# Performance work log

Hardware: AMD Instinct MI355X
Metric: run time of the kernel (lower is better)

The kernel has to match this reference:

```python
import jax, jax.numpy as jnp
import numpy as np

D_MODEL, D_STATE, D_CONV, EXPAND = 1024, 16, 4, 2
D_INNER = D_MODEL * EXPAND
B, L = 2, 2048


def setup_inputs() -> dict:
    key = jax.random.key(0)
    ks = jax.random.split(key, 12)
    s = lambda *sh: 1.0 / np.sqrt(sh[-1])
    x = jax.random.normal(ks[0], (B, L, D_MODEL), dtype=jnp.float32)
    W_in = jax.random.normal(ks[1], (2 * D_INNER, D_MODEL), dtype=jnp.float32) * s(D_MODEL)
    conv_w = jax.random.normal(ks[2], (D_INNER, 1, D_CONV), dtype=jnp.float32) * s(D_CONV)
    conv_b = jax.random.normal(ks[3], (D_INNER,), dtype=jnp.float32) * 0.01
    W_x = jax.random.normal(ks[4], (2 * D_STATE, D_INNER), dtype=jnp.float32) * s(D_INNER)
    W_dt = jax.random.normal(ks[5], (D_INNER, D_INNER), dtype=jnp.float32) * s(D_INNER)
    b_dt = jax.random.normal(ks[6], (D_INNER,), dtype=jnp.float32) * 0.01
    A_log = jnp.log(jnp.broadcast_to(jnp.arange(1, D_STATE + 1, dtype=jnp.float32)[None, :], (D_INNER, D_STATE)))
    Dp = jnp.ones((D_INNER,), dtype=jnp.float32)
    W_out = jax.random.normal(ks[7], (D_MODEL, D_INNER), dtype=jnp.float32) * s(D_INNER)
    ln_g = jnp.ones((D_MODEL,), dtype=jnp.float32)
    ln_b = jnp.zeros((D_MODEL,), dtype=jnp.float32)
    return {"x": x, "W_in": W_in, "conv_w": conv_w, "conv_b": conv_b, "W_x": W_x,
            "W_dt": W_dt, "b_dt": b_dt, "A_log": A_log, "Dp": Dp, "W_out": W_out,
            "ln_g": ln_g, "ln_b": ln_b}


def _layernorm(x, g, b, eps=1e-5):
    mu = jnp.mean(x, axis=-1, keepdims=True)
    var = jnp.mean(jnp.square(x - mu), axis=-1, keepdims=True)
    return (x - mu) * jax.lax.rsqrt(var + eps) * g + b


def _silu(x):
    return x * jax.nn.sigmoid(x)


def _ssm(x, A_log, Dp, W_x, W_dt, b_dt):
    # x: (B, L, D_INNER)
    A = -jnp.exp(A_log)                                  # (D, N)
    x_dbl = jnp.einsum('bld,nd->bln', x, W_x)            # (B, L, 2N)
    B_mat, C_mat = jnp.split(x_dbl, 2, axis=-1)          # (B, L, N) each
    dt = jax.nn.softplus(jnp.einsum('bld,ed->ble', x, W_dt) + b_dt)  # (B, L, D)

    def step(h, inp):
        dt_t, B_t, C_t, x_t = inp                        # (B,D),(B,N),(B,N),(B,D)
        A_bar = jnp.exp(dt_t[..., None] * A)             # (B, D, N)
        h = A_bar * h + (dt_t * x_t)[..., None] * B_t[:, None, :]
        y_t = jnp.einsum('bdn,bn->bd', h, C_t)
        return h, y_t

    h0 = jnp.zeros((x.shape[0], D_INNER, D_STATE), dtype=x.dtype)
    xs = (jnp.swapaxes(dt, 0, 1), jnp.swapaxes(B_mat, 0, 1),
          jnp.swapaxes(C_mat, 0, 1), jnp.swapaxes(x, 0, 1))
    _, ys = jax.lax.scan(step, h0, xs)                   # ys: (L, B, D)
    y = jnp.swapaxes(ys, 0, 1)
    return y + Dp * x


def reference(x, W_in, conv_w, conv_b, W_x, W_dt, b_dt, A_log, Dp, W_out, ln_g, ln_b):
    residual = x
    xn = _layernorm(x, ln_g, ln_b)
    xz = jnp.einsum('bld,ed->ble', xn, W_in)             # (B, L, 2*D_INNER)
    x_branch, z = jnp.split(xz, 2, axis=-1)
    # causal depthwise conv1d (torch pads both sides then truncates to L == left pad)
    x_c = jax.lax.conv_general_dilated(
        jnp.swapaxes(x_branch, 1, 2), conv_w,
        window_strides=(1,), padding=[(D_CONV - 1, 0)],
        dimension_numbers=('NCH', 'OIH', 'NCH'),
        feature_group_count=D_INNER) + conv_b[None, :, None]
    x_branch = _silu(jnp.swapaxes(x_c, 1, 2))
    y = _ssm(x_branch, A_log, Dp, W_x, W_dt, b_dt)
    y = y * _silu(z)
    return jnp.einsum('bld,md->blm', y, W_out) + residual
```

## Files before the change

kernel.cpp:

```cpp
#include <hip/hip_runtime.h>
#include <math.h>

#define D_MODEL 1024
#define D_STATE 16
#define D_INNER 2048
#define BATCH 2
#define SEQ 2048
#define ROWS (BATCH * SEQ)
#define NCAT (D_INNER + 2 * D_STATE)

#define CHUNK 32
#define NCH (SEQ / CHUNK)

typedef __bf16 bf16x8 __attribute__((ext_vector_type(8)));
typedef float f32x4 __attribute__((ext_vector_type(4)));

__device__ __forceinline__ unsigned short f2bf(float f) {
    unsigned u = __float_as_uint(f);
    u += 0x7FFF + ((u >> 16) & 1);
    return (unsigned short)(u >> 16);
}
__device__ __forceinline__ float bf2f(unsigned short s) {
    return __uint_as_float((unsigned)s << 16);
}
__device__ __forceinline__ float fast_softplus(float x) {
    return x > 15.f ? x : __logf(1.f + __expf(x));
}

__global__ __launch_bounds__(256) void ln_kernel(const float* __restrict__ x,
                                                 const float* __restrict__ g,
                                                 const float* __restrict__ b,
                                                 unsigned short* __restrict__ out) {
    int r = blockIdx.x;
    int t = threadIdx.x;
    const float* xr = x + (size_t)r * D_MODEL;
    float4 v = *(const float4*)(xr + t * 4);
    float s  = v.x + v.y + v.z + v.w;
    float ss = v.x * v.x + v.y * v.y + v.z * v.z + v.w * v.w;
    for (int off = 32; off > 0; off >>= 1) {
        s  += __shfl_down(s, off);
        ss += __shfl_down(ss, off);
    }
    __shared__ float ws[8], wss[8];
    int wid = t >> 6, lane = t & 63;
    if (lane == 0) { ws[wid] = s; wss[wid] = ss; }
    __syncthreads();
    if (t == 0) {
        float S = 0.f, SS = 0.f;
        for (int i = 0; i < 4; ++i) { S += ws[i]; SS += wss[i]; }
        float mu = S * (1.f / D_MODEL);
        float var = SS * (1.f / D_MODEL) - mu * mu;
        ws[4] = mu;
        ws[5] = rsqrtf(var + 1e-5f);
    }
    __syncthreads();
    float mu = ws[4], rs = ws[5];
    float4 gv = *(const float4*)(g + t * 4);
    float4 bv = *(const float4*)(b + t * 4);
    ushort4 o;
    o.x = f2bf((v.x - mu) * rs * gv.x + bv.x);
    o.y = f2bf((v.y - mu) * rs * gv.y + bv.y);
    o.z = f2bf((v.z - mu) * rs * gv.z + bv.z);
    o.w = f2bf((v.w - mu) * rs * gv.w + bv.w);
    ((ushort4*)(out + (size_t)r * D_MODEL))[t] = o;
}

#define N4_WIN  (2 * D_INNER * D_MODEL / 4)
#define N4_WDT  (D_INNER * D_INNER / 4)
#define N4_WX   (2 * D_STATE * D_INNER / 4)
#define N4_WOUT (D_MODEL * D_INNER / 4)
#define N4_ALL  (N4_WIN + N4_WDT + N4_WX + N4_WOUT)

__global__ __launch_bounds__(256) void cast_weights(const float* __restrict__ W_in,
                                                    const float* __restrict__ W_dt,
                                                    const float* __restrict__ W_x,
                                                    const float* __restrict__ W_out,
                                                    unsigned short* __restrict__ Win_b,
                                                    unsigned short* __restrict__ Wcat_b,
                                                    unsigned short* __restrict__ Wout_b) {
    int i = blockIdx.x * 256 + threadIdx.x;
    const float* src;
    unsigned short* dst;
    int j = i;
    if (j < N4_WIN) { src = W_in; dst = Win_b; }
    else if ((j -= N4_WIN) < N4_WDT) { src = W_dt; dst = Wcat_b; }
    else if ((j -= N4_WDT) < N4_WX)  { src = W_x;  dst = Wcat_b + (size_t)D_INNER * D_INNER; }
    else if ((j -= N4_WX) < N4_WOUT) { src = W_out; dst = Wout_b; }
    else return;
    float4 v = ((const float4*)src)[j];
    ushort4 o;
    o.x = f2bf(v.x); o.y = f2bf(v.y); o.z = f2bf(v.z); o.w = f2bf(v.w);
    ((ushort4*)dst)[j] = o;
}

template <bool BF16_OUT>
__global__ __launch_bounds__(256) void gemm_mfma(const unsigned short* __restrict__ A,
                                                 const unsigned short* __restrict__ Bw,
                                                 void* __restrict__ Cv,
                                                 const float* __restrict__ resid,
                                                 int M, int N, int K, int nby) {
    __shared__ unsigned short As[2][128 * 32];
    __shared__ unsigned short Bs[2][128 * 32];
    const int t = threadIdx.x;
    const int wave = t >> 6, lane = t & 63;
    const int bx = blockIdx.x / nby, by = blockIdx.x % nby;
    const int bm = by * 128, bn = bx * 128;
    const int wm = (wave >> 1) * 64, wn = (wave & 1) * 64;

    const int srow0 = 32 * wave;
    const int sr = lane >> 2;
    const int ss = lane & 3;
    const int sc = ss ^ ((sr >> 1) & 3);

    const int mrow = lane & 15, q = lane >> 4;
    const int rslot = q ^ ((mrow >> 1) & 3);

    f32x4 acc[4][4] = {};

    for (int k0 = 0; k0 < K; k0 += 64) {
#pragma unroll
        for (int h = 0; h < 2; ++h) {
#pragma unroll
            for (int j = 0; j < 2; ++j) {
                int r = srow0 + 16 * j + sr;
                const unsigned short* ga = A + (size_t)(bm + r) * K + k0 + 32 * h + sc * 8;
                __builtin_amdgcn_global_load_lds(
                    (const __attribute__((address_space(1))) void*)ga,
                    (__attribute__((address_space(3))) void*)&As[h][(srow0 + 16 * j) * 32],
                    16, 0, 0);
                int nr = bn + r; if (nr > N - 1) nr = N - 1;
                const unsigned short* gb = Bw + (size_t)nr * K + k0 + 32 * h + sc * 8;
                __builtin_amdgcn_global_load_lds(
                    (const __attribute__((address_space(1))) void*)gb,
                    (__attribute__((address_space(3))) void*)&Bs[h][(srow0 + 16 * j) * 32],
                    16, 0, 0);
            }
        }
        __syncthreads();
#pragma unroll
        for (int h = 0; h < 2; ++h) {
            bf16x8 a[4], b[4];
            const bf16x8* Av = (const bf16x8*)As[h];
            const bf16x8* Bv = (const bf16x8*)Bs[h];
#pragma unroll
            for (int i = 0; i < 4; ++i) a[i] = Av[(wm + i * 16 + mrow) * 4 + rslot];
#pragma unroll
            for (int j = 0; j < 4; ++j) b[j] = Bv[(wn + j * 16 + mrow) * 4 + rslot];
#pragma unroll
            for (int i = 0; i < 4; ++i)
#pragma unroll
                for (int j = 0; j < 4; ++j)
                    acc[i][j] = __builtin_amdgcn_mfma_f32_16x16x32_bf16(a[i], b[j], acc[i][j], 0, 0, 0);
        }
        __syncthreads();
    }

#pragma unroll
    for (int j = 0; j < 4; ++j) {
        int col = bn + wn + j * 16 + mrow;
        if (col < N) {
#pragma unroll
            for (int i = 0; i < 4; ++i) {
                int rowb = bm + wm + i * 16 + q * 4;
#pragma unroll
                for (int r = 0; r < 4; ++r) {
                    size_t idx = (size_t)(rowb + r) * N + col;
                    float v = acc[i][j][r];
                    if (BF16_OUT) {
                        ((unsigned short*)Cv)[idx] = f2bf(v);
                    } else {
                        if (resid) v += resid[idx];
                        ((float*)Cv)[idx] = v;
                    }
                }
            }
        }
    }
}

__global__ __launch_bounds__(256) void conv_silu(const unsigned short* __restrict__ xz_b,
                                                 const float* __restrict__ cw,
                                                 const float* __restrict__ cb,
                                                 unsigned short* __restrict__ out_b) {
    int idx = blockIdx.x * 256 + threadIdx.x;
    int d4 = (idx & (D_INNER / 4 - 1)) * 4;
    int r = idx >> 9;
    int l = r & (SEQ - 1);
    const unsigned short* base = xz_b + (size_t)r * (2 * D_INNER) + d4;
    float4 b4 = *(const float4*)(cb + d4);
    float acc[4] = {b4.x, b4.y, b4.z, b4.w};
    ushort4 xq[4];
#pragma unroll
    for (int j = 0; j < 4; ++j)
        if (l >= 3 - j) xq[j] = *(const ushort4*)(base - (size_t)(3 - j) * (2 * D_INNER));
#pragma unroll
    for (int i = 0; i < 4; ++i) {
        float4 w = *(const float4*)(cw + (size_t)(d4 + i) * 4);
        const float* wp = (const float*)&w;
#pragma unroll
        for (int j = 0; j < 4; ++j) {
            if (l >= 3 - j) {
                unsigned short q = (&xq[j].x)[i];
                acc[i] = fmaf(wp[j], bf2f(q), acc[i]);
            }
        }
    }
    ushort4 o;
#pragma unroll
    for (int i = 0; i < 4; ++i) {
        float sv = acc[i] / (1.f + __expf(-acc[i]));
        (&o.x)[i] = f2bf(sv);
    }
    *(ushort4*)(out_b + (size_t)r * D_INNER + d4) = o;
}

__global__ __launch_bounds__(256) void scan_pass1(const float* __restrict__ dtcat,
                                                  const unsigned short* __restrict__ xconv_b,
                                                  const float* __restrict__ b_dt,
                                                  float* __restrict__ hfin,
                                                  float* __restrict__ Ssum) {
    int blk = blockIdx.x;
    int dblk = blk & 7;
    int b = (blk >> 3) & (BATCH - 1);
    int c = blk >> 4;
    int t = threadIdx.x;
    int d = dblk * 256 + t;
    int r0 = b * SEQ + c * CHUNK;

    __shared__ float bcs[CHUNK][32];
    {
        int row = t >> 3, f4 = t & 7;
        const float4* src = (const float4*)(dtcat + (size_t)(r0 + row) * NCAT + D_INNER);
        *(float4*)&bcs[row][f4 * 4] = src[f4];
    }
    __syncthreads();

    float h[D_STATE] = {};
    float S = 0.f;
    float bdt = b_dt[d];
    float dtp = dtcat[(size_t)r0 * NCAT + d];
    unsigned short xq = xconv_b[(size_t)r0 * D_INNER + d];
    for (int l = 0; l < CHUNK; ++l) {
        float dtp_n = 0.f; unsigned short xq_n = 0;
        if (l + 1 < CHUNK) {
            dtp_n = dtcat[(size_t)(r0 + l + 1) * NCAT + d];
            xq_n = xconv_b[(size_t)(r0 + l + 1) * D_INNER + d];
        }
        float dtv = fast_softplus(dtp + bdt);
        S += dtv;
        float dtx = dtv * bf2f(xq);
        float w = __expf(-dtv);
        float ab = 1.f;
#pragma unroll
        for (int n = 0; n < D_STATE; ++n) {
            ab *= w;
            h[n] = fmaf(ab, h[n], dtx * bcs[l][n]);
        }
        dtp = dtp_n; xq = xq_n;
    }
    size_t cb = ((size_t)c * BATCH + b);
#pragma unroll
    for (int n = 0; n < D_STATE; ++n)
        hfin[(cb * D_STATE + n) * D_INNER + d] = h[n];
    Ssum[cb * D_INNER + d] = S;
}

__global__ __launch_bounds__(256) void scan_pass2(const float* __restrict__ hfin,
                                                  const float* __restrict__ Ssum,
                                                  const float* __restrict__ A_log,
                                                  float* __restrict__ Hinit) {
    int tid = blockIdx.x * 256 + threadIdx.x;
    int d = tid & (D_INNER - 1);
    int n = (tid >> 11) & (D_STATE - 1);
    int b = tid >> 15;
    float Ac = -__expf(A_log[(size_t)d * D_STATE + n]);
    float H = 0.f;
    for (int c = 0; c < NCH; ++c) {
        size_t cb = ((size_t)c * BATCH + b);
        size_t idx = (cb * D_STATE + n) * D_INNER + d;
        Hinit[idx] = H;
        float s = Ssum[cb * D_INNER + d];
        H = fmaf(__expf(Ac * s), H, hfin[idx]);
    }
}

__global__ __launch_bounds__(256) void scan_pass3(const float* __restrict__ dtcat,
                                                  const unsigned short* __restrict__ xconv_b,
                                                  const unsigned short* __restrict__ xz_b,
                                                  const float* __restrict__ b_dt,
                                                  const float* __restrict__ Dp,
                                                  const float* __restrict__ Hinit,
                                                  unsigned short* __restrict__ y_b) {
    int blk = blockIdx.x;
    int dblk = blk & 7;
    int b = (blk >> 3) & (BATCH - 1);
    int c = blk >> 4;
    int t = threadIdx.x;
    int d = dblk * 256 + t;
    int r0 = b * SEQ + c * CHUNK;

    __shared__ float bcs[CHUNK][32];
    {
        int row = t >> 3, f4 = t & 7;
        const float4* src = (const float4*)(dtcat + (size_t)(r0 + row) * NCAT + D_INNER);
        *(float4*)&bcs[row][f4 * 4] = src[f4];
    }
    __syncthreads();

    float h[D_STATE];
    size_t cb = ((size_t)c * BATCH + b);
#pragma unroll
    for (int n = 0; n < D_STATE; ++n)
        h[n] = Hinit[(cb * D_STATE + n) * D_INNER + d];
    float bdt = b_dt[d];
    float dp = Dp[d];
    float dtp = dtcat[(size_t)r0 * NCAT + d];
    unsigned short xq = xconv_b[(size_t)r0 * D_INNER + d];
    unsigned short zq = xz_b[(size_t)r0 * (2 * D_INNER) + D_INNER + d];
    for (int l = 0; l < CHUNK; ++l) {
        int r = r0 + l;
        float dtp_n = 0.f; unsigned short xq_n = 0, zq_n = 0;
        if (l + 1 < CHUNK) {
            dtp_n = dtcat[(size_t)(r + 1) * NCAT + d];
            xq_n = xconv_b[(size_t)(r + 1) * D_INNER + d];
            zq_n = xz_b[(size_t)(r + 1) * (2 * D_INNER) + D_INNER + d];
        }
        float dtv = fast_softplus(dtp + bdt);
        float xv = bf2f(xq);
        float dtx = dtv * xv;
        float w = __expf(-dtv);
        float ab = 1.f;
        float y = 0.f;
#pragma unroll
        for (int n = 0; n < D_STATE; ++n) {
            ab *= w;
            h[n] = fmaf(ab, h[n], dtx * bcs[l][n]);
            y = fmaf(h[n], bcs[l][D_STATE + n], y);
        }
        y = fmaf(dp, xv, y);
        float zv = bf2f(zq);
        float sz = zv / (1.f + __expf(-zv));
        y_b[(size_t)r * D_INNER + d] = f2bf(y * sz);
        dtp = dtp_n; xq = xq_n; zq = zq_n;
    }
}

extern "C" void kernel_launch(void* const* d_in, const int* in_sizes, int n_in,
                              void* d_out, int out_size, void* d_ws, size_t ws_size,
                              hipStream_t stream) {
    const float* x      = (const float*)d_in[0];
    const float* W_in   = (const float*)d_in[1];
    const float* conv_w = (const float*)d_in[2];
    const float* conv_b = (const float*)d_in[3];
    const float* W_x    = (const float*)d_in[4];
    const float* W_dt   = (const float*)d_in[5];
    const float* b_dt   = (const float*)d_in[6];
    const float* A_log  = (const float*)d_in[7];
    const float* Dp     = (const float*)d_in[8];
    const float* W_out  = (const float*)d_in[9];
    const float* ln_g   = (const float*)d_in[10];
    const float* ln_b   = (const float*)d_in[11];
    float* out = (float*)d_out;

    unsigned short* xz_b = (unsigned short*)d_ws;
    float* dtcat = (float*)(xz_b + (size_t)ROWS * 2 * D_INNER);
    unsigned short* xn_b    = (unsigned short*)(dtcat + (size_t)ROWS * NCAT);
    unsigned short* Win_b   = xn_b   + (size_t)2 * D_INNER * D_MODEL;
    unsigned short* Wcat_b  = Win_b  + (size_t)2 * D_INNER * D_MODEL;
    unsigned short* Wout_b  = Wcat_b + (size_t)NCAT * D_INNER;
    unsigned short* xconv_b = Wout_b + (size_t)D_MODEL * D_INNER;
    unsigned short* y_b     = xconv_b;
    float* hfin  = (float*)(xconv_b + (size_t)ROWS * D_INNER);
    float* Hinit = hfin + (size_t)NCH * BATCH * D_STATE * D_INNER;
    float* Ssum  = Hinit + (size_t)NCH * BATCH * D_STATE * D_INNER;

    cast_weights<<<(N4_ALL + 255) / 256, 256, 0, stream>>>(
        W_in, W_dt, W_x, W_out, Win_b, Wcat_b, Wout_b);
    ln_kernel<<<ROWS, 256, 0, stream>>>(x, ln_g, ln_b, xn_b);

    gemm_mfma<true><<<32 * 32, 256, 0, stream>>>(xn_b, Win_b, xz_b, nullptr,
                                                 ROWS, 2 * D_INNER, D_MODEL, 32);

    conv_silu<<<(ROWS * D_INNER / 4) / 256, 256, 0, stream>>>(xz_b, conv_w, conv_b, xconv_b);

    gemm_mfma<false><<<17 * 32, 256, 0, stream>>>(xconv_b, Wcat_b, dtcat, nullptr,
                                                  ROWS, NCAT, D_INNER, 32);

    scan_pass1<<<NCH * BATCH * 8, 256, 0, stream>>>(dtcat, xconv_b, b_dt, hfin, Ssum);
    scan_pass2<<<(BATCH * D_STATE * D_INNER) / 256, 256, 0, stream>>>(hfin, Ssum, A_log, Hinit);
    scan_pass3<<<NCH * BATCH * 8, 256, 0, stream>>>(dtcat, xconv_b, xz_b, b_dt, Dp, Hinit, y_b);

    gemm_mfma<false><<<8 * 32, 256, 0, stream>>>(y_b, Wout_b, out, x,
                                                 ROWS, D_MODEL, D_INNER, 32);
}
```

Before: 375.8 us.

## Register-prefetch double-buffered GEMM pipeline and merge weight cast with layernorm

New measurement: 682.1 us. 1.82x slower.

```diff
diff --git a/kernel.cpp b/kernel.cpp
--- a/kernel.cpp
+++ b/kernel.cpp
@@ -27,12 +27,42 @@
     return x > 15.f ? x : __logf(1.f + __expf(x));
 }
 
-__global__ __launch_bounds__(256) void ln_kernel(const float* __restrict__ x,
-                                                 const float* __restrict__ g,
-                                                 const float* __restrict__ b,
-                                                 unsigned short* __restrict__ out) {
-    int r = blockIdx.x;
+#define N4_WIN  (2 * D_INNER * D_MODEL / 4)
+#define N4_WDT  (D_INNER * D_INNER / 4)
+#define N4_WX   (2 * D_STATE * D_INNER / 4)
+#define N4_WOUT (D_MODEL * D_INNER / 4)
+#define N4_ALL  (N4_WIN + N4_WDT + N4_WX + N4_WOUT)
+#define NCAST_BLK (N4_ALL / 256)
+
+__global__ __launch_bounds__(256) void cast_ln(const float* __restrict__ W_in,
+                                               const float* __restrict__ W_dt,
+                                               const float* __restrict__ W_x,
+                                               const float* __restrict__ W_out,
+                                               unsigned short* __restrict__ Win_b,
+                                               unsigned short* __restrict__ Wcat_b,
+                                               unsigned short* __restrict__ Wout_b,
+                                               const float* __restrict__ x,
+                                               const float* __restrict__ g,
+                                               const float* __restrict__ b,
+                                               unsigned short* __restrict__ xn_b) {
+    __shared__ float ws[8], wss[8];
     int t = threadIdx.x;
+    if (blockIdx.x < NCAST_BLK) {
+        int i = blockIdx.x * 256 + t;
+        const float* src;
+        unsigned short* dst;
+        int j = i;
+        if (j < N4_WIN) { src = W_in; dst = Win_b; }
+        else if ((j -= N4_WIN) < N4_WDT) { src = W_dt; dst = Wcat_b; }
+        else if ((j -= N4_WDT) < N4_WX)  { src = W_x;  dst = Wcat_b + (size_t)D_INNER * D_INNER; }
+        else { j -= N4_WX; src = W_out; dst = Wout_b; }
+        float4 v = ((const float4*)src)[j];
+        ushort4 o;
+        o.x = f2bf(v.x); o.y = f2bf(v.y); o.z = f2bf(v.z); o.w = f2bf(v.w);
+        ((ushort4*)dst)[j] = o;
+        return;
+    }
+    int r = blockIdx.x - NCAST_BLK;
     const float* xr = x + (size_t)r * D_MODEL;
     float4 v = *(const float4*)(xr + t * 4);
     float s  = v.x + v.y + v.z + v.w;
@@ -41,7 +71,6 @@
         s  += __shfl_down(s, off);
         ss += __shfl_down(ss, off);
     }
-    __shared__ float ws[8], wss[8];
     int wid = t >> 6, lane = t & 63;
     if (lane == 0) { ws[wid] = s; wss[wid] = ss; }
     __syncthreads();
@@ -62,35 +91,7 @@
     o.y = f2bf((v.y - mu) * rs * gv.y + bv.y);
     o.z = f2bf((v.z - mu) * rs * gv.z + bv.z);
     o.w = f2bf((v.w - mu) * rs * gv.w + bv.w);
-    ((ushort4*)(out + (size_t)r * D_MODEL))[t] = o;
-}
-
-#define N4_WIN  (2 * D_INNER * D_MODEL / 4)
-#define N4_WDT  (D_INNER * D_INNER / 4)
-#define N4_WX   (2 * D_STATE * D_INNER / 4)
-#define N4_WOUT (D_MODEL * D_INNER / 4)
-#define N4_ALL  (N4_WIN + N4_WDT + N4_WX + N4_WOUT)
-
-__global__ __launch_bounds__(256) void cast_weights(const float* __restrict__ W_in,
-                                                    const float* __restrict__ W_dt,
-                                                    const float* __restrict__ W_x,
-                                                    const float* __restrict__ W_out,
-                                                    unsigned short* __restrict__ Win_b,
-                                                    unsigned short* __restrict__ Wcat_b,
-                                                    unsigned short* __restrict__ Wout_b) {
-    int i = blockIdx.x * 256 + threadIdx.x;
-    const float* src;
-    unsigned short* dst;
-    int j = i;
-    if (j < N4_WIN) { src = W_in; dst = Win_b; }
-    else if ((j -= N4_WIN) < N4_WDT) { src = W_dt; dst = Wcat_b; }
-    else if ((j -= N4_WDT) < N4_WX)  { src = W_x;  dst = Wcat_b + (size_t)D_INNER * D_INNER; }
-    else if ((j -= N4_WX) < N4_WOUT) { src = W_out; dst = Wout_b; }
-    else return;
-    float4 v = ((const float4*)src)[j];
-    ushort4 o;
-    o.x = f2bf(v.x); o.y = f2bf(v.y); o.z = f2bf(v.z); o.w = f2bf(v.w);
-    ((ushort4*)dst)[j] = o;
+    ((ushort4*)(xn_b + (size_t)r * D_MODEL))[t] = o;
 }
 
 template <bool BF16_OUT>
@@ -99,8 +100,8 @@
                                                  void* __restrict__ Cv,
                                                  const float* __restrict__ resid,
                                                  int M, int N, int K, int nby) {
-    __shared__ unsigned short As[2][128 * 32];
-    __shared__ unsigned short Bs[2][128 * 32];
+    __shared__ __align__(16) unsigned short As[2][2][128 * 32];
+    __shared__ __align__(16) unsigned short Bs[2][2][128 * 32];
     const int t = threadIdx.x;
     const int wave = t >> 6, lane = t & 63;
     const int bx = blockIdx.x / nby, by = blockIdx.x % nby;
@@ -115,33 +116,41 @@
     const int mrow = lane & 15, q = lane >> 4;
     const int rslot = q ^ ((mrow >> 1) & 3);
 
+    const unsigned short* Ab = A + (size_t)(bm + srow0 + sr) * K + sc * 8;
+    const size_t arow = (size_t)16 * K;
+    int nr0 = bn + srow0 + sr;      if (nr0 > N - 1) nr0 = N - 1;
+    int nr1 = bn + srow0 + 16 + sr; if (nr1 > N - 1) nr1 = N - 1;
+    const unsigned short* Bb0 = Bw + (size_t)nr0 * K + sc * 8;
+    const unsigned short* Bb1 = Bw + (size_t)nr1 * K + sc * 8;
+
+    uint4 ra[2][8];
+
+    auto load = [&](int set, int k0) {
+#pragma unroll
+        for (int h = 0; h < 2; ++h) {
+            ra[set][h * 2 + 0] = *(const uint4*)(Ab + k0 + 32 * h);
+            ra[set][h * 2 + 1] = *(const uint4*)(Ab + arow + k0 + 32 * h);
+            ra[set][4 + h * 2 + 0] = *(const uint4*)(Bb0 + k0 + 32 * h);
+            ra[set][4 + h * 2 + 1] = *(const uint4*)(Bb1 + k0 + 32 * h);
+        }
+    };
+    auto store = [&](int set, int buf) {
+#pragma unroll
+        for (int h = 0; h < 2; ++h)
+#pragma unroll
+            for (int j = 0; j < 2; ++j) {
+                *(uint4*)(&As[buf][h][(srow0 + 16 * j) * 32 + lane * 8]) = ra[set][h * 2 + j];
+                *(uint4*)(&Bs[buf][h][(srow0 + 16 * j) * 32 + lane * 8]) = ra[set][4 + h * 2 + j];
+            }
+    };
+
     f32x4 acc[4][4] = {};
-
-    for (int k0 = 0; k0 < K; k0 += 64) {
-#pragma unroll
-        for (int h = 0; h < 2; ++h) {
-#pragma unroll
-            for (int j = 0; j < 2; ++j) {
-                int r = srow0 + 16 * j + sr;
-                const unsigned short* ga = A + (size_t)(bm + r) * K + k0 + 32 * h + sc * 8;
-                __builtin_amdgcn_global_load_lds(
-                    (const __attribute__((address_space(1))) void*)ga,
-                    (__attribute__((address_space(3))) void*)&As[h][(srow0 + 16 * j) * 32],
-                    16, 0, 0);
-                int nr = bn + r; if (nr > N - 1) nr = N - 1;
-                const unsigned short* gb = Bw + (size_t)nr * K + k0 + 32 * h + sc * 8;
-                __builtin_amdgcn_global_load_lds(
-                    (const __attribute__((address_space(1))) void*)gb,
-                    (__attribute__((address_space(3))) void*)&Bs[h][(srow0 + 16 * j) * 32],
-                    16, 0, 0);
-            }
-        }
-        __syncthreads();
+    auto compute = [&](int buf) {
 #pragma unroll
         for (int h = 0; h < 2; ++h) {
             bf16x8 a[4], b[4];
-            const bf16x8* Av = (const bf16x8*)As[h];
-            const bf16x8* Bv = (const bf16x8*)Bs[h];
+            const bf16x8* Av = (const bf16x8*)As[buf][h];
+            const bf16x8* Bv = (const bf16x8*)Bs[buf][h];
 #pragma unroll
             for (int i = 0; i < 4; ++i) a[i] = Av[(wm + i * 16 + mrow) * 4 + rslot];
 #pragma unroll
@@ -151,6 +160,26 @@
 #pragma unroll
                 for (int j = 0; j < 4; ++j)
                     acc[i][j] = __builtin_amdgcn_mfma_f32_16x16x32_bf16(a[i], b[j], acc[i][j], 0, 0, 0);
+        }
+    };
+
+    const int nk = K >> 6;
+    load(0, 0);
+    store(0, 0);
+    load(1, 64);
+    __syncthreads();
+
+    for (int i = 0; i < nk; i += 2) {
+        compute(0);
+        {
+            store(1, 1);
+            if (i + 2 < nk) load(0, (i + 2) << 6);
+        }
+        __syncthreads();
+        compute(1);
+        if (i + 2 < nk) {
+            store(0, 0);
+            if (i + 3 < nk) load(1, (i + 3) << 6);
         }
         __syncthreads();
     }
@@ -200,8 +229,8 @@
 #pragma unroll
         for (int j = 0; j < 4; ++j) {
             if (l >= 3 - j) {
-                unsigned short q = (&xq[j].x)[i];
-                acc[i] = fmaf(wp[j], bf2f(q), acc[i]);
+                unsigned short qv = (&xq[j].x)[i];
+                acc[i] = fmaf(wp[j], bf2f(qv), acc[i]);
             }
         }
     }
@@ -374,9 +403,8 @@
     float* Hinit = hfin + (size_t)NCH * BATCH * D_STATE * D_INNER;
     float* Ssum  = Hinit + (size_t)NCH * BATCH * D_STATE * D_INNER;
 
-    cast_weights<<<(N4_ALL + 255) / 256, 256, 0, stream>>>(
-        W_in, W_dt, W_x, W_out, Win_b, Wcat_b, Wout_b);
-    ln_kernel<<<ROWS, 256, 0, stream>>>(x, ln_g, ln_b, xn_b);
+    cast_ln<<<NCAST_BLK + ROWS, 256, 0, stream>>>(
+        W_in, W_dt, W_x, W_out, Win_b, Wcat_b, Wout_b, x, ln_g, ln_b, xn_b);
 
     gemm_mfma<true><<<32 * 32, 256, 0, stream>>>(xn_b, Win_b, xz_b, nullptr,
                                                  ROWS, 2 * D_INNER, D_MODEL, 32);
```

## Merge weight cast with layernorm and add register-prefetch pipelined GEMM for dt projection

Applied to the files above, without the earlier changes.

Result: slower. 537.2 us (+43.0%).

```diff
diff --git a/kernel.cpp b/kernel.cpp
--- a/kernel.cpp
+++ b/kernel.cpp
@@ -27,12 +27,42 @@
     return x > 15.f ? x : __logf(1.f + __expf(x));
 }
 
-__global__ __launch_bounds__(256) void ln_kernel(const float* __restrict__ x,
-                                                 const float* __restrict__ g,
-                                                 const float* __restrict__ b,
-                                                 unsigned short* __restrict__ out) {
-    int r = blockIdx.x;
+#define N4_WIN  (2 * D_INNER * D_MODEL / 4)
+#define N4_WDT  (D_INNER * D_INNER / 4)
+#define N4_WX   (2 * D_STATE * D_INNER / 4)
+#define N4_WOUT (D_MODEL * D_INNER / 4)
+#define N4_ALL  (N4_WIN + N4_WDT + N4_WX + N4_WOUT)
+#define NCAST_BLK (N4_ALL / 256)
+
+__global__ __launch_bounds__(256) void cast_ln(const float* __restrict__ W_in,
+                                               const float* __restrict__ W_dt,
+                                               const float* __restrict__ W_x,
+                                               const float* __restrict__ W_out,
+                                               unsigned short* __restrict__ Win_b,
+                                               unsigned short* __restrict__ Wcat_b,
+                                               unsigned short* __restrict__ Wout_b,
+                                               const float* __restrict__ x,
+                                               const float* __restrict__ g,
+                                               const float* __restrict__ b,
+                                               unsigned short* __restrict__ xn_b) {
+    __shared__ float ws[8], wss[8];
     int t = threadIdx.x;
+    if (blockIdx.x < NCAST_BLK) {
+        int i = blockIdx.x * 256 + t;
+        const float* src;
+        unsigned short* dst;
+        int j = i;
+        if (j < N4_WIN) { src = W_in; dst = Win_b; }
+        else if ((j -= N4_WIN) < N4_WDT) { src = W_dt; dst = Wcat_b; }
+        else if ((j -= N4_WDT) < N4_WX)  { src = W_x;  dst = Wcat_b + (size_t)D_INNER * D_INNER; }
+        else { j -= N4_WX; src = W_out; dst = Wout_b; }
+        float4 v = ((const float4*)src)[j];
+        ushort4 o;
+        o.x = f2bf(v.x); o.y = f2bf(v.y); o.z = f2bf(v.z); o.w = f2bf(v.w);
+        ((ushort4*)dst)[j] = o;
+        return;
+    }
+    int r = blockIdx.x - NCAST_BLK;
     const float* xr = x + (size_t)r * D_MODEL;
     float4 v = *(const float4*)(xr + t * 4);
     float s  = v.x + v.y + v.z + v.w;
@@ -41,7 +71,6 @@
         s  += __shfl_down(s, off);
         ss += __shfl_down(ss, off);
     }
-    __shared__ float ws[8], wss[8];
     int wid = t >> 6, lane = t & 63;
     if (lane == 0) { ws[wid] = s; wss[wid] = ss; }
     __syncthreads();
@@ -62,43 +91,15 @@
     o.y = f2bf((v.y - mu) * rs * gv.y + bv.y);
     o.z = f2bf((v.z - mu) * rs * gv.z + bv.z);
     o.w = f2bf((v.w - mu) * rs * gv.w + bv.w);
-    ((ushort4*)(out + (size_t)r * D_MODEL))[t] = o;
-}
-
-#define N4_WIN  (2 * D_INNER * D_MODEL / 4)
-#define N4_WDT  (D_INNER * D_INNER / 4)
-#define N4_WX   (2 * D_STATE * D_INNER / 4)
-#define N4_WOUT (D_MODEL * D_INNER / 4)
-#define N4_ALL  (N4_WIN + N4_WDT + N4_WX + N4_WOUT)
-
-__global__ __launch_bounds__(256) void cast_weights(const float* __restrict__ W_in,
-                                                    const float* __restrict__ W_dt,
-                                                    const float* __restrict__ W_x,
-                                                    const float* __restrict__ W_out,
-                                                    unsigned short* __restrict__ Win_b,
-                                                    unsigned short* __restrict__ Wcat_b,
-                                                    unsigned short* __restrict__ Wout_b) {
-    int i = blockIdx.x * 256 + threadIdx.x;
-    const float* src;
-    unsigned short* dst;
-    int j = i;
-    if (j < N4_WIN) { src = W_in; dst = Win_b; }
-    else if ((j -= N4_WIN) < N4_WDT) { src = W_dt; dst = Wcat_b; }
-    else if ((j -= N4_WDT) < N4_WX)  { src = W_x;  dst = Wcat_b + (size_t)D_INNER * D_INNER; }
-    else if ((j -= N4_WX) < N4_WOUT) { src = W_out; dst = Wout_b; }
-    else return;
-    float4 v = ((const float4*)src)[j];
-    ushort4 o;
-    o.x = f2bf(v.x); o.y = f2bf(v.y); o.z = f2bf(v.z); o.w = f2bf(v.w);
-    ((ushort4*)dst)[j] = o;
+    ((ushort4*)(xn_b + (size_t)r * D_MODEL))[t] = o;
 }
 
 template <bool BF16_OUT>
-__global__ __launch_bounds__(256) void gemm_mfma(const unsigned short* __restrict__ A,
-                                                 const unsigned short* __restrict__ Bw,
-                                                 void* __restrict__ Cv,
-                                                 const float* __restrict__ resid,
-                                                 int M, int N, int K, int nby) {
+__global__ __launch_bounds__(256) void gemm_dma(const unsigned short* __restrict__ A,
+                                                const unsigned short* __restrict__ Bw,
+                                                void* __restrict__ Cv,
+                                                const float* __restrict__ resid,
+                                                int M, int N, int K, int nby) {
     __shared__ unsigned short As[2][128 * 32];
     __shared__ unsigned short Bs[2][128 * 32];
     const int t = threadIdx.x;
@@ -178,6 +179,119 @@
     }
 }
 
+#define GLOAD(rs, k0)                                                   \
+    {                                                                   \
+        _Pragma("unroll")                                               \
+        for (int h = 0; h < 2; ++h) {                                   \
+            rs[h * 2 + 0] = *(const uint4*)(Ab + (k0) + 32 * h);        \
+            rs[h * 2 + 1] = *(const uint4*)(Ab + arow + (k0) + 32 * h); \
+            rs[4 + h * 2 + 0] = *(const uint4*)(Bb0 + (k0) + 32 * h);   \
+            rs[4 + h * 2 + 1] = *(const uint4*)(Bb1 + (k0) + 32 * h);   \
+        }                                                               \
+    }
+
+#define SSTORE(rs, buf)                                                           \
+    {                                                                             \
+        _Pragma("unroll")                                                         \
+        for (int h = 0; h < 2; ++h) {                                             \
+            *(uint4*)(&As[buf][h][(srow0) * 32 + lane * 8]) = rs[h * 2 + 0];      \
+            *(uint4*)(&As[buf][h][(srow0 + 16) * 32 + lane * 8]) = rs[h * 2 + 1]; \
+            *(uint4*)(&Bs[buf][h][(srow0) * 32 + lane * 8]) = rs[4 + h * 2 + 0];  \
+            *(uint4*)(&Bs[buf][h][(srow0 + 16) * 32 + lane * 8]) = rs[4 + h * 2 + 1]; \
+        }                                                                         \
+    }
+
+#define COMPUTE(buf)                                                              \
+    {                                                                             \
+        _Pragma("unroll")                                                         \
+        for (int h = 0; h < 2; ++h) {                                             \
+            bf16x8 a[4], b[4];                                                    \
+            const bf16x8* Av = (const bf16x8*)As[buf][h];                         \
+            const bf16x8* Bv = (const bf16x8*)Bs[buf][h];                         \
+            _Pragma("unroll")                                                     \
+            for (int i = 0; i < 4; ++i) a[i] = Av[(wm + i * 16 + mrow) * 4 + rslot]; \
+            _Pragma("unroll")                                                     \
+            for (int j = 0; j < 4; ++j) b[j] = Bv[(wn + j * 16 + mrow) * 4 + rslot]; \
+            _Pragma("unroll")                                                     \
+            for (int i = 0; i < 4; ++i)                                           \
+                _Pragma("unroll")                                                 \
+                for (int j = 0; j < 4; ++j)                                       \
+                    acc[i][j] = __builtin_amdgcn_mfma_f32_16x16x32_bf16(a[i], b[j], acc[i][j], 0, 0, 0); \
+        }                                                                         \
+    }
+
+template <bool BF16_OUT>
+__global__ __launch_bounds__(256, 2) void gemm_pipe(const unsigned short* __restrict__ A,
+                                                    const unsigned short* __restrict__ Bw,
+                                                    void* __restrict__ Cv,
+                                                    const float* __restrict__ resid,
+                                                    int M, int N, int K, int nby) {
+    __shared__ __align__(16) unsigned short As[2][2][128 * 32];
+    __shared__ __align__(16) unsigned short Bs[2][2][128 * 32];
+    const int t = threadIdx.x;
+    const int wave = t >> 6, lane = t & 63;
+    const int bx = blockIdx.x / nby, by = blockIdx.x % nby;
+    const int bm = by * 128, bn = bx * 128;
+    const int wm = (wave >> 1) * 64, wn = (wave & 1) * 64;
+
+    const int srow0 = 32 * wave;
+    const int sr = lane >> 2;
+    const int ss = lane & 3;
+    const int sc = ss ^ ((sr >> 1) & 3);
+
+    const int mrow = lane & 15, q = lane >> 4;
+    const int rslot = q ^ ((mrow >> 1) & 3);
+
+    const unsigned short* Ab = A + (size_t)(bm + srow0 + sr) * K + sc * 8;
+    const size_t arow = (size_t)16 * K;
+    int nr0 = bn + srow0 + sr;      if (nr0 > N - 1) nr0 = N - 1;
+    int nr1 = bn + srow0 + 16 + sr; if (nr1 > N - 1) nr1 = N - 1;
+    const unsigned short* Bb0 = Bw + (size_t)nr0 * K + sc * 8;
+    const unsigned short* Bb1 = Bw + (size_t)nr1 * K + sc * 8;
+
+    uint4 r0[8], r1[8];
+    f32x4 acc[4][4] = {};
+
+    const int nk = K >> 6;
+    GLOAD(r0, 0)
+    SSTORE(r0, 0)
+    GLOAD(r1, 64)
+    __syncthreads();
+
+    for (int i = 0; i < nk; i += 2) {
+        if (i + 2 < nk) GLOAD(r0, (i + 2) << 6)
+        COMPUTE(0)
+        SSTORE(r1, 1)
+        __syncthreads();
+        if (i + 3 < nk) GLOAD(r1, (i + 3) << 6)
+        COMPUTE(1)
+        if (i + 2 < nk) SSTORE(r0, 0)
+        __syncthreads();
+    }
+
+#pragma unroll
+    for (int j = 0; j < 4; ++j) {
+        int col = bn + wn + j * 16 + mrow;
+        if (col < N) {
+#pragma unroll
+            for (int i = 0; i < 4; ++i) {
+                int rowb = bm + wm + i * 16 + q * 4;
+#pragma unroll
+                for (int r = 0; r < 4; ++r) {
+                    size_t idx = (size_t)(rowb + r) * N + col;
+                    float v = acc[i][j][r];
+                    if (BF16_OUT) {
+                        ((unsigned short*)Cv)[idx] = f2bf(v);
+                    } else {
+                        if (resid) v += resid[idx];
+                        ((float*)Cv)[idx] = v;
+                    }
+                }
+            }
+        }
+    }
+}
+
 __global__ __launch_bounds__(256) void conv_silu(const unsigned short* __restrict__ xz_b,
                                                  const float* __restrict__ cw,
                                                  const float* __restrict__ cb,
@@ -200,8 +314,8 @@
 #pragma unroll
         for (int j = 0; j < 4; ++j) {
             if (l >= 3 - j) {
-                unsigned short q = (&xq[j].x)[i];
-                acc[i] = fmaf(wp[j], bf2f(q), acc[i]);
+                unsigned short qv = (&xq[j].x)[i];
+                acc[i] = fmaf(wp[j], bf2f(qv), acc[i]);
             }
         }
     }
@@ -374,22 +488,21 @@
     float* Hinit = hfin + (size_t)NCH * BATCH * D_STATE * D_INNER;
     float* Ssum  = Hinit + (size_t)NCH * BATCH * D_STATE * D_INNER;
 
-    cast_weights<<<(N4_ALL + 255) / 256, 256, 0, stream>>>(
-        W_in, W_dt, W_x, W_out, Win_b, Wcat_b, Wout_b);
-    ln_kernel<<<ROWS, 256, 0, stream>>>(x, ln_g, ln_b, xn_b);
-
-    gemm_mfma<true><<<32 * 32, 256, 0, stream>>>(xn_b, Win_b, xz_b, nullptr,
-                                                 ROWS, 2 * D_INNER, D_MODEL, 32);
+    cast_ln<<<NCAST_BLK + ROWS, 256, 0, stream>>>(
+        W_in, W_dt, W_x, W_out, Win_b, Wcat_b, Wout_b, x, ln_g, ln_b, xn_b);
+
+    gemm_dma<true><<<32 * 32, 256, 0, stream>>>(xn_b, Win_b, xz_b, nullptr,
+                                                ROWS, 2 * D_INNER, D_MODEL, 32);
 
     conv_silu<<<(ROWS * D_INNER / 4) / 256, 256, 0, stream>>>(xz_b, conv_w, conv_b, xconv_b);
 
-    gemm_mfma<false><<<17 * 32, 256, 0, stream>>>(xconv_b, Wcat_b, dtcat, nullptr,
+    gemm_pipe<false><<<17 * 32, 256, 0, stream>>>(xconv_b, Wcat_b, dtcat, nullptr,
                                                   ROWS, NCAT, D_INNER, 32);
 
     scan_pass1<<<NCH * BATCH * 8, 256, 0, stream>>>(dtcat, xconv_b, b_dt, hfin, Ssum);
     scan_pass2<<<(BATCH * D_STATE * D_INNER) / 256, 256, 0, stream>>>(hfin, Ssum, A_log, Hinit);
     scan_pass3<<<NCH * BATCH * 8, 256, 0, stream>>>(dtcat, xconv_b, xz_b, b_dt, Dp, Hinit, y_b);
 
-    gemm_mfma<false><<<8 * 32, 256, 0, stream>>>(y_b, Wout_b, out, x,
-                                                 ROWS, D_MODEL, D_INNER, 32);
-}
+    gemm_dma<false><<<8 * 32, 256, 0, stream>>>(y_b, Wout_b, out, x,
+                                                ROWS, D_MODEL, D_INNER, 32);
+}
```

## Merge weight cast with layernorm and store dt projection in bf16

Applied to the files above, without the earlier changes.

Result: no change. 369.8 us (-1.6%).

```diff
diff --git a/kernel.cpp b/kernel.cpp
--- a/kernel.cpp
+++ b/kernel.cpp
@@ -27,12 +27,42 @@
     return x > 15.f ? x : __logf(1.f + __expf(x));
 }
 
-__global__ __launch_bounds__(256) void ln_kernel(const float* __restrict__ x,
-                                                 const float* __restrict__ g,
-                                                 const float* __restrict__ b,
-                                                 unsigned short* __restrict__ out) {
-    int r = blockIdx.x;
+#define N4_WIN  (2 * D_INNER * D_MODEL / 4)
+#define N4_WDT  (D_INNER * D_INNER / 4)
+#define N4_WX   (2 * D_STATE * D_INNER / 4)
+#define N4_WOUT (D_MODEL * D_INNER / 4)
+#define N4_ALL  (N4_WIN + N4_WDT + N4_WX + N4_WOUT)
+#define NCAST_BLK (N4_ALL / 256)
+
+__global__ __launch_bounds__(256) void cast_ln(const float* __restrict__ W_in,
+                                               const float* __restrict__ W_dt,
+                                               const float* __restrict__ W_x,
+                                               const float* __restrict__ W_out,
+                                               unsigned short* __restrict__ Win_b,
+                                               unsigned short* __restrict__ Wcat_b,
+                                               unsigned short* __restrict__ Wout_b,
+                                               const float* __restrict__ x,
+                                               const float* __restrict__ g,
+                                               const float* __restrict__ b,
+                                               unsigned short* __restrict__ xn_b) {
+    __shared__ float ws[8], wss[8];
     int t = threadIdx.x;
+    if (blockIdx.x < NCAST_BLK) {
+        int i = blockIdx.x * 256 + t;
+        const float* src;
+        unsigned short* dst;
+        int j = i;
+        if (j < N4_WIN) { src = W_in; dst = Win_b; }
+        else if ((j -= N4_WIN) < N4_WDT) { src = W_dt; dst = Wcat_b; }
+        else if ((j -= N4_WDT) < N4_WX)  { src = W_x;  dst = Wcat_b + (size_t)D_INNER * D_INNER; }
+        else { j -= N4_WX; src = W_out; dst = Wout_b; }
+        float4 v = ((const float4*)src)[j];
+        ushort4 o;
+        o.x = f2bf(v.x); o.y = f2bf(v.y); o.z = f2bf(v.z); o.w = f2bf(v.w);
+        ((ushort4*)dst)[j] = o;
+        return;
+    }
+    int r = blockIdx.x - NCAST_BLK;
     const float* xr = x + (size_t)r * D_MODEL;
     float4 v = *(const float4*)(xr + t * 4);
     float s  = v.x + v.y + v.z + v.w;
@@ -41,7 +71,6 @@
         s  += __shfl_down(s, off);
         ss += __shfl_down(ss, off);
     }
-    __shared__ float ws[8], wss[8];
     int wid = t >> 6, lane = t & 63;
     if (lane == 0) { ws[wid] = s; wss[wid] = ss; }
     __syncthreads();
@@ -62,43 +91,15 @@
     o.y = f2bf((v.y - mu) * rs * gv.y + bv.y);
     o.z = f2bf((v.z - mu) * rs * gv.z + bv.z);
     o.w = f2bf((v.w - mu) * rs * gv.w + bv.w);
-    ((ushort4*)(out + (size_t)r * D_MODEL))[t] = o;
-}
-
-#define N4_WIN  (2 * D_INNER * D_MODEL / 4)
-#define N4_WDT  (D_INNER * D_INNER / 4)
-#define N4_WX   (2 * D_STATE * D_INNER / 4)
-#define N4_WOUT (D_MODEL * D_INNER / 4)
-#define N4_ALL  (N4_WIN + N4_WDT + N4_WX + N4_WOUT)
-
-__global__ __launch_bounds__(256) void cast_weights(const float* __restrict__ W_in,
-                                                    const float* __restrict__ W_dt,
-                                                    const float* __restrict__ W_x,
-                                                    const float* __restrict__ W_out,
-                                                    unsigned short* __restrict__ Win_b,
-                                                    unsigned short* __restrict__ Wcat_b,
-                                                    unsigned short* __restrict__ Wout_b) {
-    int i = blockIdx.x * 256 + threadIdx.x;
-    const float* src;
-    unsigned short* dst;
-    int j = i;
-    if (j < N4_WIN) { src = W_in; dst = Win_b; }
-    else if ((j -= N4_WIN) < N4_WDT) { src = W_dt; dst = Wcat_b; }
-    else if ((j -= N4_WDT) < N4_WX)  { src = W_x;  dst = Wcat_b + (size_t)D_INNER * D_INNER; }
-    else if ((j -= N4_WX) < N4_WOUT) { src = W_out; dst = Wout_b; }
-    else return;
-    float4 v = ((const float4*)src)[j];
-    ushort4 o;
-    o.x = f2bf(v.x); o.y = f2bf(v.y); o.z = f2bf(v.z); o.w = f2bf(v.w);
-    ((ushort4*)dst)[j] = o;
-}
-
-template <bool BF16_OUT>
-__global__ __launch_bounds__(256) void gemm_mfma(const unsigned short* __restrict__ A,
-                                                 const unsigned short* __restrict__ Bw,
-                                                 void* __restrict__ Cv,
-                                                 const float* __restrict__ resid,
-                                                 int M, int N, int K, int nby) {
+    ((ushort4*)(xn_b + (size_t)r * D_MODEL))[t] = o;
+}
+
+template <int MODE>
+__global__ __launch_bounds__(256) void gemm_dma(const unsigned short* __restrict__ A,
+                                                const unsigned short* __restrict__ Bw,
+                                                void* __restrict__ Cv,
+                                                float* __restrict__ aux,
+                                                int M, int N, int K, int nby) {
     __shared__ unsigned short As[2][128 * 32];
     __shared__ unsigned short Bs[2][128 * 32];
     const int t = threadIdx.x;
@@ -164,13 +165,18 @@
                 int rowb = bm + wm + i * 16 + q * 4;
 #pragma unroll
                 for (int r = 0; r < 4; ++r) {
-                    size_t idx = (size_t)(rowb + r) * N + col;
                     float v = acc[i][j][r];
-                    if (BF16_OUT) {
-                        ((unsigned short*)Cv)[idx] = f2bf(v);
+                    if (MODE == 1) {
+                        ((unsigned short*)Cv)[(size_t)(rowb + r) * N + col] = f2bf(v);
+                    } else if (MODE == 0) {
+                        size_t idx = (size_t)(rowb + r) * N + col;
+                        if (aux) v += aux[idx];
+                        ((float*)Cv)[idx] = v;
                     } else {
-                        if (resid) v += resid[idx];
-                        ((float*)Cv)[idx] = v;
+                        if (col < D_INNER)
+                            ((unsigned short*)Cv)[(size_t)(rowb + r) * D_INNER + col] = f2bf(v);
+                        else
+                            aux[(size_t)(rowb + r) * (2 * D_STATE) + (col - D_INNER)] = v;
                     }
                 }
             }
@@ -200,8 +206,8 @@
 #pragma unroll
         for (int j = 0; j < 4; ++j) {
             if (l >= 3 - j) {
-                unsigned short q = (&xq[j].x)[i];
-                acc[i] = fmaf(wp[j], bf2f(q), acc[i]);
+                unsigned short qv = (&xq[j].x)[i];
+                acc[i] = fmaf(wp[j], bf2f(qv), acc[i]);
             }
         }
     }
@@ -214,7 +220,8 @@
     *(ushort4*)(out_b + (size_t)r * D_INNER + d4) = o;
 }
 
-__global__ __launch_bounds__(256) void scan_pass1(const float* __restrict__ dtcat,
+__global__ __launch_bounds__(256) void scan_pass1(const unsigned short* __restrict__ dtb,
+                                                  const float* __restrict__ xdbl,
                                                   const unsigned short* __restrict__ xconv_b,
                                                   const float* __restrict__ b_dt,
                                                   float* __restrict__ hfin,
@@ -228,25 +235,21 @@
     int r0 = b * SEQ + c * CHUNK;
 
     __shared__ float bcs[CHUNK][32];
-    {
-        int row = t >> 3, f4 = t & 7;
-        const float4* src = (const float4*)(dtcat + (size_t)(r0 + row) * NCAT + D_INNER);
-        *(float4*)&bcs[row][f4 * 4] = src[f4];
-    }
+    ((float4*)&bcs[0][0])[t] = ((const float4*)(xdbl + (size_t)r0 * (2 * D_STATE)))[t];
     __syncthreads();
 
     float h[D_STATE] = {};
     float S = 0.f;
     float bdt = b_dt[d];
-    float dtp = dtcat[(size_t)r0 * NCAT + d];
+    unsigned short dq = dtb[(size_t)r0 * D_INNER + d];
     unsigned short xq = xconv_b[(size_t)r0 * D_INNER + d];
     for (int l = 0; l < CHUNK; ++l) {
-        float dtp_n = 0.f; unsigned short xq_n = 0;
+        unsigned short dq_n = 0, xq_n = 0;
         if (l + 1 < CHUNK) {
-            dtp_n = dtcat[(size_t)(r0 + l + 1) * NCAT + d];
+            dq_n = dtb[(size_t)(r0 + l + 1) * D_INNER + d];
             xq_n = xconv_b[(size_t)(r0 + l + 1) * D_INNER + d];
         }
-        float dtv = fast_softplus(dtp + bdt);
+        float dtv = fast_softplus(bf2f(dq) + bdt);
         S += dtv;
         float dtx = dtv * bf2f(xq);
         float w = __expf(-dtv);
@@ -256,7 +259,7 @@
             ab *= w;
             h[n] = fmaf(ab, h[n], dtx * bcs[l][n]);
         }
-        dtp = dtp_n; xq = xq_n;
+        dq = dq_n; xq = xq_n;
     }
     size_t cb = ((size_t)c * BATCH + b);
 #pragma unroll
@@ -284,7 +287,8 @@
     }
 }
 
-__global__ __launch_bounds__(256) void scan_pass3(const float* __restrict__ dtcat,
+__global__ __launch_bounds__(256) void scan_pass3(const unsigned short* __restrict__ dtb,
+                                                  const float* __restrict__ xdbl,
                                                   const unsigned short* __restrict__ xconv_b,
                                                   const unsigned short* __restrict__ xz_b,
                                                   const float* __restrict__ b_dt,
@@ -300,11 +304,7 @@
     int r0 = b * SEQ + c * CHUNK;
 
     __shared__ float bcs[CHUNK][32];
-    {
-        int row = t >> 3, f4 = t & 7;
-        const float4* src = (const float4*)(dtcat + (size_t)(r0 + row) * NCAT + D_INNER);
-        *(float4*)&bcs[row][f4 * 4] = src[f4];
-    }
+    ((float4*)&bcs[0][0])[t] = ((const float4*)(xdbl + (size_t)r0 * (2 * D_STATE)))[t];
     __syncthreads();
 
     float h[D_STATE];
@@ -314,18 +314,18 @@
         h[n] = Hinit[(cb * D_STATE + n) * D_INNER + d];
     float bdt = b_dt[d];
     float dp = Dp[d];
-    float dtp = dtcat[(size_t)r0 * NCAT + d];
+    unsigned short dq = dtb[(size_t)r0 * D_INNER + d];
     unsigned short xq = xconv_b[(size_t)r0 * D_INNER + d];
     unsigned short zq = xz_b[(size_t)r0 * (2 * D_INNER) + D_INNER + d];
     for (int l = 0; l < CHUNK; ++l) {
         int r = r0 + l;
-        float dtp_n = 0.f; unsigned short xq_n = 0, zq_n = 0;
+        unsigned short dq_n = 0, xq_n = 0, zq_n = 0;
         if (l + 1 < CHUNK) {
-            dtp_n = dtcat[(size_t)(r + 1) * NCAT + d];
+            dq_n = dtb[(size_t)(r + 1) * D_INNER + d];
             xq_n = xconv_b[(size_t)(r + 1) * D_INNER + d];
             zq_n = xz_b[(size_t)(r + 1) * (2 * D_INNER) + D_INNER + d];
         }
-        float dtv = fast_softplus(dtp + bdt);
+        float dtv = fast_softplus(bf2f(dq) + bdt);
         float xv = bf2f(xq);
         float dtx = dtv * xv;
         float w = __expf(-dtv);
@@ -341,7 +341,7 @@
         float zv = bf2f(zq);
         float sz = zv / (1.f + __expf(-zv));
         y_b[(size_t)r * D_INNER + d] = f2bf(y * sz);
-        dtp = dtp_n; xq = xq_n; zq = zq_n;
+        dq = dq_n; xq = xq_n; zq = zq_n;
     }
 }
 
@@ -363,8 +363,9 @@
     float* out = (float*)d_out;
 
     unsigned short* xz_b = (unsigned short*)d_ws;
-    float* dtcat = (float*)(xz_b + (size_t)ROWS * 2 * D_INNER);
-    unsigned short* xn_b    = (unsigned short*)(dtcat + (size_t)ROWS * NCAT);
+    unsigned short* dtb  = xz_b + (size_t)ROWS * 2 * D_INNER;
+    float* xdbl = (float*)(dtb + (size_t)ROWS * D_INNER);
+    unsigned short* xn_b    = (unsigned short*)(xdbl + (size_t)ROWS * 2 * D_STATE);
     unsigned short* Win_b   = xn_b   + (size_t)2 * D_INNER * D_MODEL;
     unsigned short* Wcat_b  = Win_b  + (size_t)2 * D_INNER * D_MODEL;
     unsigned short* Wout_b  = Wcat_b + (size_t)NCAT * D_INNER;
@@ -374,22 +375,21 @@
     float* Hinit = hfin + (size_t)NCH * BATCH * D_STATE * D_INNER;
     float* Ssum  = Hinit + (size_t)NCH * BATCH * D_STATE * D_INNER;
 
-    cast_weights<<<(N4_ALL + 255) / 256, 256, 0, stream>>>(
-        W_in, W_dt, W_x, W_out, Win_b, Wcat_b, Wout_b);
-    ln_kernel<<<ROWS, 256, 0, stream>>>(x, ln_g, ln_b, xn_b);
-
-    gemm_mfma<true><<<32 * 32, 256, 0, stream>>>(xn_b, Win_b, xz_b, nullptr,
-                                                 ROWS, 2 * D_INNER, D_MODEL, 32);
+    cast_ln<<<NCAST_BLK + ROWS, 256, 0, stream>>>(
+        W_in, W_dt, W_x, W_out, Win_b, Wcat_b, Wout_b, x, ln_g, ln_b, xn_b);
+
+    gemm_dma<1><<<32 * 32, 256, 0, stream>>>(xn_b, Win_b, xz_b, nullptr,
+                                             ROWS, 2 * D_INNER, D_MODEL, 32);
 
     conv_silu<<<(ROWS * D_INNER / 4) / 256, 256, 0, stream>>>(xz_b, conv_w, conv_b, xconv_b);
 
-    gemm_mfma<false><<<17 * 32, 256, 0, stream>>>(xconv_b, Wcat_b, dtcat, nullptr,
-                                                  ROWS, NCAT, D_INNER, 32);
-
-    scan_pass1<<<NCH * BATCH * 8, 256, 0, stream>>>(dtcat, xconv_b, b_dt, hfin, Ssum);
+    gemm_dma<2><<<17 * 32, 256, 0, stream>>>(xconv_b, Wcat_b, dtb, xdbl,
+                                             ROWS, NCAT, D_INNER, 32);
+
+    scan_pass1<<<NCH * BATCH * 8, 256, 0, stream>>>(dtb, xdbl, xconv_b, b_dt, hfin, Ssum);
     scan_pass2<<<(BATCH * D_STATE * D_INNER) / 256, 256, 0, stream>>>(hfin, Ssum, A_log, Hinit);
-    scan_pass3<<<NCH * BATCH * 8, 256, 0, stream>>>(dtcat, xconv_b, xz_b, b_dt, Dp, Hinit, y_b);
-
-    gemm_mfma<false><<<8 * 32, 256, 0, stream>>>(y_b, Wout_b, out, x,
-                                                 ROWS, D_MODEL, D_INNER, 32);
-}
+    scan_pass3<<<NCH * BATCH * 8, 256, 0, stream>>>(dtb, xdbl, xconv_b, xz_b, b_dt, Dp, Hinit, y_b);
+
+    gemm_dma<0><<<8 * 32, 256, 0, stream>>>(y_b, Wout_b, out, (float*)x,
+                                            ROWS, D_MODEL, D_INNER, 32);
+}
```
